# Optimization experiments

Hardware: AMD Instinct MI355X
Metric: run time of the kernel (lower is better)

## Reference

```python
import jax, jax.numpy as jnp
import numpy as np

B = 8
N_GENES = 19836
D_IN = 11
D_H = 64
DEG = 16
N = B * N_GENES
E_PER = N_GENES * DEG


def setup_inputs() -> dict:
    key = jax.random.key(0)
    ks = jax.random.split(key, 20)
    x = jax.random.normal(ks[0], (B, N_GENES, D_IN), dtype=jnp.float32)
    # edges: random within each graph, offset by graph index
    base_src = jax.random.randint(ks[1], (B, E_PER), 0, N_GENES)
    base_dst = jax.random.randint(ks[2], (B, E_PER), 0, N_GENES)
    offs = (jnp.arange(B) * N_GENES)[:, None]
    src = (base_src + offs).reshape(-1).astype(jnp.int64) if False else (base_src + offs).reshape(-1)
    dst = (base_dst + offs).reshape(-1)
    s = 0.02
    def nrm(k, shape):
        return jax.random.normal(k, shape, dtype=jnp.float32) * s
    return {
        'x': x, 'src': src, 'dst': dst,
        'enc_W': nrm(ks[3], (D_H, D_IN)), 'enc_b': jnp.zeros((D_H,), jnp.float32),
        'gene_emb': nrm(ks[4], (N_GENES, D_H)),
        'gin_W': nrm(ks[5], (D_H, D_H)),
        'bn_w': 1.0 + nrm(ks[6], (D_H,)), 'bn_b': jnp.zeros((D_H,), jnp.float32),
        'key_W': nrm(ks[7], (D_H, D_H)), 'key_b': jnp.zeros((D_H,), jnp.float32),
        'query_w': nrm(ks[8], (1, D_H)),
        'val_W': nrm(ks[9], (D_H, D_H)), 'val_b': jnp.zeros((D_H,), jnp.float32),
        'sae_enc_W': nrm(ks[10], (D_H, D_H)), 'sae_enc_b': jnp.zeros((D_H,), jnp.float32),
        'sae_dec_W': nrm(ks[11], (D_H, D_H)), 'sae_dec_b': jnp.zeros((D_H,), jnp.float32),
        'pred_W1': nrm(ks[12], (D_H, D_H)), 'pred_b1': jnp.zeros((D_H,), jnp.float32),
        'pred_W2': nrm(ks[13], (1, D_H)), 'pred_b2': jnp.zeros((1,), jnp.float32),
    }


def gelu(x):
    return jax.nn.gelu(x, approximate=False)  # nn.GELU default = exact erf


def batchnorm(h, w, b, eps=1e-5):
    # training-mode BatchNorm1d: batch statistics, biased variance
    mu = jnp.mean(h, axis=0)
    var = jnp.mean((h - mu) ** 2, axis=0)
    return (h - mu) * jax.lax.rsqrt(var + eps) * w + b


def reference(x, src, dst, enc_W, enc_b, gene_emb, gin_W, bn_w, bn_b,
              key_W, key_b, query_w, val_W, val_b,
              sae_enc_W, sae_enc_b, sae_dec_W, sae_dec_b,
              pred_W1, pred_b1, pred_W2, pred_b2):
    bsz, n_gene, d_in = x.shape
    n_nodes = bsz * n_gene
    # gene encoder: single Linear (bias) + GELU (inner batchnorm result is discarded in source)
    h = gelu(x.reshape(-1, d_in) @ enc_W.T + enc_b)          # [N, D_H]
    h = (h.reshape(bsz, n_gene, -1) + gene_emb).reshape(n_nodes, -1)
    # GIN layer (eps=0, sum aggregation): MLP(h + sum_{u->v} h_u); MLP = single Linear, no bias
    agg = jax.ops.segment_sum(h[src], dst, num_segments=n_nodes)  # irregular gather/scatter
    h = (h + agg) @ gin_W.T
    h = gelu(batchnorm(h, bn_w, bn_b))
    # attentive readout with SAE
    keys = h @ key_W.T + key_b
    w = jax.nn.sigmoid(keys @ query_w.T)                     # [N, 1]
    v = h @ val_W.T + val_b
    z = v * w
    enc = jax.nn.relu(z @ sae_enc_W.T + sae_enc_b)
    dec = enc @ sae_dec_W.T + sae_dec_b
    sae_loss = jnp.mean((dec - z) ** 2) + 1.0 * jnp.mean(jnp.abs(enc))
    gid = jnp.arange(n_nodes) // n_gene
    g_h = jax.ops.segment_sum(dec * w, gid, num_segments=bsz)  # [B, D_H]
    # predictor: Linear+GELU, Linear (inner batchnorm discarded in source)
    preds = gelu(g_h @ pred_W1.T + pred_b1) @ pred_W2.T + pred_b2
    return preds, w, sae_loss, dec
```

## Files before the change

kernel.cpp:

```cpp
#include <hip/hip_runtime.h>
#include <hip/hip_bf16.h>
#include <math.h>

#define NGENES 19836
#define BATCH 8
#define DIN 11
#define DH 64
#define NNODES (BATCH * NGENES)
#define E_PER (NGENES * 16)
#define NEDGES (NNODES * 16)
#define NDH (NNODES * DH)
#define NWAVE ((NNODES + 63) / 64)
#define NBLK_NODE ((NWAVE + 3) / 4)

#define SCAN_CHUNK 1024
#define NSBLK ((NNODES + SCAN_CHUNK - 1) / SCAN_CHUNK)

#define OUT_PREDS 0
#define OUT_W 8
#define OUT_SAE (8 + NNODES)
#define OUT_DEC (9 + NNODES)

__device__ __forceinline__ float gelu_f(float x) {
    return 0.5f * x * (1.0f + erff(x * 0.70710678118654752f));
}

__device__ __forceinline__ float bcast(float v, int lane) {
    return __int_as_float(__builtin_amdgcn_readlane(__float_as_int(v), lane));
}

__device__ __forceinline__ float wave_sum(float v) {
    #pragma unroll
    for (int o = 32; o; o >>= 1) v += __shfl_xor(v, o, 64);
    return v;
}

__global__ void k_encoder(const float* __restrict__ x, const float* __restrict__ encW,
                          const float* __restrict__ encB, const float* __restrict__ gemb,
                          __hip_bfloat16* __restrict__ h16) {
    int lane = threadIdx.x & 63;
    int g = blockIdx.x & 7;
    int wix = (blockIdx.x >> 3) * (blockDim.x >> 6) + (threadIdx.x >> 6);
    int wper = (gridDim.x >> 3) * (blockDim.x >> 6);
    float wreg[DIN];
    #pragma unroll
    for (int k = 0; k < DIN; ++k) wreg[k] = encW[lane * DIN + k];
    float bias = encB[lane];
    size_t gb = (size_t)g * NGENES;
    for (int i = wix; i < NGENES; i += wper) {
        size_t node = gb + i;
        const float* xr = x + node * DIN;
        float acc = bias;
        #pragma unroll
        for (int k = 0; k < DIN; ++k) acc = fmaf(xr[k], wreg[k], acc);
        float hv = gelu_f(acc) + gemb[(size_t)i * DH + lane];
        h16[node * DH + lane] = __float2bfloat16(hv);
    }
}

__global__ void k_hist(const int* __restrict__ dst, int* __restrict__ counts) {
    int g = blockIdx.x & 7;
    int t = (blockIdx.x >> 3) * blockDim.x + threadIdx.x;
    int nt = (gridDim.x >> 3) * blockDim.x;
    const int* dg = dst + (size_t)g * E_PER;
    for (int e = t; e < E_PER; e += nt)
        atomicAdd(&counts[dg[e]], 1);
}

__global__ void k_scan1(const int* __restrict__ counts, int* __restrict__ bsum) {
    __shared__ int red[256];
    int base = blockIdx.x * SCAN_CHUNK + threadIdx.x * 4;
    int s = 0;
    #pragma unroll
    for (int i = 0; i < 4; ++i) {
        int n = base + i;
        if (n < NNODES) s += counts[n];
    }
    red[threadIdx.x] = s;
    __syncthreads();
    for (int o = 128; o; o >>= 1) {
        if (threadIdx.x < o) red[threadIdx.x] += red[threadIdx.x + o];
        __syncthreads();
    }
    if (threadIdx.x == 0) bsum[blockIdx.x] = red[0];
}

__global__ void k_scan2(const int* __restrict__ bsum, int* __restrict__ boff) {
    __shared__ int red[256];
    int t = threadIdx.x;
    int v = (t < NSBLK) ? bsum[t] : 0;
    red[t] = v;
    __syncthreads();
    for (int o = 1; o < 256; o <<= 1) {
        int u = (t >= o) ? red[t - o] : 0;
        __syncthreads();
        red[t] += u;
        __syncthreads();
    }
    if (t < NSBLK) boff[t] = red[t] - v;
}

__global__ void k_scan3(const int* __restrict__ counts, const int* __restrict__ boff,
                        int* __restrict__ offsets, int* __restrict__ cursor) {
    __shared__ int red[256];
    int t = threadIdx.x;
    int base = blockIdx.x * SCAN_CHUNK + t * 4;
    int c[4];
    int s = 0;
    #pragma unroll
    for (int i = 0; i < 4; ++i) {
        int n = base + i;
        c[i] = (n < NNODES) ? counts[n] : 0;
        s += c[i];
    }
    red[t] = s;
    __syncthreads();
    for (int o = 1; o < 256; o <<= 1) {
        int v = (t >= o) ? red[t - o] : 0;
        __syncthreads();
        red[t] += v;
        __syncthreads();
    }
    int excl = red[t] - s + boff[blockIdx.x];
    #pragma unroll
    for (int i = 0; i < 4; ++i) {
        int n = base + i;
        if (n < NNODES) { offsets[n] = excl; cursor[n] = excl; }
        excl += c[i];
    }
}

__global__ void k_scatter(const int* __restrict__ src, const int* __restrict__ dst,
                          int* __restrict__ cursor, unsigned short* __restrict__ csr) {
    int g = blockIdx.x & 7;
    int t = (blockIdx.x >> 3) * blockDim.x + threadIdx.x;
    int nt = (gridDim.x >> 3) * blockDim.x;
    const int* sg = src + (size_t)g * E_PER;
    const int* dg = dst + (size_t)g * E_PER;
    int gbase = g * NGENES;
    for (int e = t; e < E_PER; e += nt) {
        int p = atomicAdd(&cursor[dg[e]], 1);
        csr[p] = (unsigned short)(sg[e] - gbase);
    }
}

__global__ void __launch_bounds__(256, 4)
k_aggin(const __hip_bfloat16* __restrict__ h16, const int* __restrict__ offsets,
        const int* __restrict__ counts, const unsigned short* __restrict__ csr,
        const float* __restrict__ ginW, float* __restrict__ h2,
        float* __restrict__ stats) {
    __shared__ float ldsW[DH * DH];
    __shared__ float red[2][256];
    for (int idx = threadIdx.x; idx < DH * DH; idx += 256) {
        int k = idx >> 6, d = idx & 63;
        ldsW[idx] = ginW[d * DH + k];
    }
    __syncthreads();
    int lane = threadIdx.x & 63;
    int g = blockIdx.x & 7;
    int wix = (blockIdx.x >> 3) * 4 + (threadIdx.x >> 6);
    int wper = (gridDim.x >> 3) * 4;
    int gbase = g * NGENES;
    float s1 = 0.f, s2 = 0.f;
    for (int i = wix; i < NGENES; i += wper) {
        int node = gbase + i;
        float a[8];
        a[0] = __bfloat162float(h16[(size_t)node * DH + lane]);
        #pragma unroll
        for (int u = 1; u < 8; ++u) a[u] = 0.f;
        int start = offsets[node];
        int cnt = counts[node];
        for (int e0 = 0; e0 < cnt; e0 += 64) {
            int nn = min(64, cnt - e0);
            int iv = (lane < nn) ? (int)csr[start + e0 + lane] : 0;
            int j = 0;
            for (; j + 7 < nn; j += 8) {
                #pragma unroll
                for (int u = 0; u < 8; ++u) {
                    int v = gbase + __shfl(iv, j + u, 64);
                    a[u] += __bfloat162float(h16[(size_t)v * DH + lane]);
                }
            }
            for (; j < nn; ++j)
                a[0] += __bfloat162float(h16[(size_t)(gbase + __shfl(iv, j, 64)) * DH + lane]);
        }
        float tval = ((a[0] + a[1]) + (a[2] + a[3])) + ((a[4] + a[5]) + (a[6] + a[7]));
        float m0 = 0.f, m1 = 0.f, m2 = 0.f, m3 = 0.f;
        #pragma unroll
        for (int k = 0; k < DH; k += 4) {
            m0 = fmaf(ldsW[(k + 0) * DH + lane], bcast(tval, k + 0), m0);
            m1 = fmaf(ldsW[(k + 1) * DH + lane], bcast(tval, k + 1), m1);
            m2 = fmaf(ldsW[(k + 2) * DH + lane], bcast(tval, k + 2), m2);
            m3 = fmaf(ldsW[(k + 3) * DH + lane], bcast(tval, k + 3), m3);
        }
        float outv = (m0 + m1) + (m2 + m3);
        h2[(size_t)node * DH + lane] = outv;
        s1 += outv;
        s2 += outv * outv;
    }
    red[0][threadIdx.x] = s1;
    red[1][threadIdx.x] = s2;
    __syncthreads();
    if (threadIdx.x < 64) {
        float t1 = red[0][threadIdx.x] + red[0][threadIdx.x + 64] + red[0][threadIdx.x + 128] + red[0][threadIdx.x + 192];
        float t2 = red[1][threadIdx.x] + red[1][threadIdx.x + 64] + red[1][threadIdx.x + 128] + red[1][threadIdx.x + 192];
        atomicAdd(&stats[threadIdx.x], t1);
        atomicAdd(&stats[64 + threadIdx.x], t2);
    }
}

__global__ void k_bnparams(const float* __restrict__ stats, const float* __restrict__ bnw,
                           const float* __restrict__ bnb, const float* __restrict__ keyW,
                           const float* __restrict__ keyB, const float* __restrict__ qw,
                           float* __restrict__ bnp) {
    int d = threadIdx.x;
    float inv_n = 1.0f / (float)NNODES;
    float mu = stats[d] * inv_n;
    float var = stats[64 + d] * inv_n - mu * mu;
    float sc = bnw[d] * rsqrtf(var + 1e-5f);
    bnp[d] = sc;
    bnp[64 + d] = bnb[d] - mu * sc;
    float kq0 = 0.f, kq1 = 0.f;
    #pragma unroll
    for (int j = 0; j < DH; j += 2) {
        kq0 = fmaf(qw[j], keyW[j * DH + d], kq0);
        kq1 = fmaf(qw[j + 1], keyW[(j + 1) * DH + d], kq1);
    }
    bnp[128 + d] = kq0 + kq1;
    float qb = wave_sum(qw[d] * keyB[d]);
    if (d == 0) bnp[192] = qb;
}

__global__ void __launch_bounds__(256, 2)
k_attn(float* __restrict__ h2, const float* __restrict__ bnp,
       const float* __restrict__ valW, const float* __restrict__ valB,
       float* __restrict__ wout) {
    int lane = threadIdx.x & 63;
    int wv = (blockIdx.x * blockDim.x + threadIdx.x) >> 6;
    int node = wv * 64 + lane;
    if (node >= NNODES) return;
    float* row = h2 + (size_t)node * DH;
    float h3[DH];
    #pragma unroll
    for (int j = 0; j < 16; ++j) {
        float4 v = *reinterpret_cast<const float4*>(row + j * 4);
        h3[j * 4] = v.x; h3[j * 4 + 1] = v.y; h3[j * 4 + 2] = v.z; h3[j * 4 + 3] = v.w;
    }
    float p = bnp[192];
    #pragma unroll
    for (int k = 0; k < DH; ++k) {
        h3[k] = gelu_f(fmaf(h3[k], bnp[k], bnp[64 + k]));
        p = fmaf(h3[k], bnp[128 + k], p);
    }
    float wq = 1.0f / (1.0f + expf(-p));
    wout[node] = wq;
    #pragma unroll 1
    for (int d4 = 0; d4 < DH; d4 += 4) {
        float a0 = valB[d4], a1 = valB[d4 + 1], a2 = valB[d4 + 2], a3 = valB[d4 + 3];
        #pragma unroll
        for (int k = 0; k < DH; ++k) {
            a0 = fmaf(valW[(d4 + 0) * DH + k], h3[k], a0);
            a1 = fmaf(valW[(d4 + 1) * DH + k], h3[k], a1);
            a2 = fmaf(valW[(d4 + 2) * DH + k], h3[k], a2);
            a3 = fmaf(valW[(d4 + 3) * DH + k], h3[k], a3);
        }
        float4 v = { a0 * wq, a1 * wq, a2 * wq, a3 * wq };
        *reinterpret_cast<float4*>(row + d4) = v;
    }
}

__global__ void __launch_bounds__(256, 2)
k_saenc(const float* __restrict__ zbuf, const float* __restrict__ encW,
        const float* __restrict__ encB, float* __restrict__ encout,
        float* __restrict__ loss) {
    int lane = threadIdx.x & 63;
    int wv = (blockIdx.x * blockDim.x + threadIdx.x) >> 6;
    int node = wv * 64 + lane;
    bool act = node < NNODES;
    const float* zr = zbuf + (size_t)node * DH;
    float z[DH];
    if (act) {
        #pragma unroll
        for (int j = 0; j < 16; ++j) {
            float4 v = *reinterpret_cast<const float4*>(zr + j * 4);
            z[j * 4] = v.x; z[j * 4 + 1] = v.y; z[j * 4 + 2] = v.z; z[j * 4 + 3] = v.w;
        }
    } else {
        #pragma unroll
        for (int k = 0; k < DH; ++k) z[k] = 0.f;
    }
    float l1 = 0.f;
    float* er = encout + (size_t)node * DH;
    #pragma unroll 1
    for (int d4 = 0; d4 < DH; d4 += 4) {
        float a0 = encB[d4], a1 = encB[d4 + 1], a2 = encB[d4 + 2], a3 = encB[d4 + 3];
        #pragma unroll
        for (int k = 0; k < DH; ++k) {
            a0 = fmaf(encW[(d4 + 0) * DH + k], z[k], a0);
            a1 = fmaf(encW[(d4 + 1) * DH + k], z[k], a1);
            a2 = fmaf(encW[(d4 + 2) * DH + k], z[k], a2);
            a3 = fmaf(encW[(d4 + 3) * DH + k], z[k], a3);
        }
        a0 = fmaxf(a0, 0.f); a1 = fmaxf(a1, 0.f);
        a2 = fmaxf(a2, 0.f); a3 = fmaxf(a3, 0.f);
        l1 += (a0 + a1) + (a2 + a3);
        if (act) {
            float4 v = { a0, a1, a2, a3 };
            *reinterpret_cast<float4*>(er + d4) = v;
        }
    }
    if (!act) l1 = 0.f;
    l1 = wave_sum(l1);
    if (lane == 0) atomicAdd(&loss[1], l1);
}

__global__ void __launch_bounds__(256, 2)
k_saedec(const float* __restrict__ zbuf, const float* __restrict__ decW,
         const float* __restrict__ decB, float* __restrict__ decout,
         float* __restrict__ loss) {
    int lane = threadIdx.x & 63;
    int wv = (blockIdx.x * blockDim.x + threadIdx.x) >> 6;
    int node = wv * 64 + lane;
    bool act = node < NNODES;
    float* dr = decout + (size_t)node * DH;
    const float* zr = zbuf + (size_t)node * DH;
    float enc[DH];
    if (act) {
        #pragma unroll
        for (int j = 0; j < 16; ++j) {
            float4 v = *reinterpret_cast<const float4*>(dr + j * 4);
            enc[j * 4] = v.x; enc[j * 4 + 1] = v.y; enc[j * 4 + 2] = v.z; enc[j * 4 + 3] = v.w;
        }
    } else {
        #pragma unroll
        for (int k = 0; k < DH; ++k) enc[k] = 0.f;
    }
    float sq = 0.f;
    #pragma unroll 1
    for (int d4 = 0; d4 < DH; d4 += 4) {
        float a0 = decB[d4], a1 = decB[d4 + 1], a2 = decB[d4 + 2], a3 = decB[d4 + 3];
        #pragma unroll
        for (int k = 0; k < DH; ++k) {
            a0 = fmaf(decW[(d4 + 0) * DH + k], enc[k], a0);
            a1 = fmaf(decW[(d4 + 1) * DH + k], enc[k], a1);
            a2 = fmaf(decW[(d4 + 2) * DH + k], enc[k], a2);
            a3 = fmaf(decW[(d4 + 3) * DH + k], enc[k], a3);
        }
        if (act) {
            float4 zv = *reinterpret_cast<const float4*>(zr + d4);
            float d0 = a0 - zv.x, d1 = a1 - zv.y, d2 = a2 - zv.z, d3 = a3 - zv.w;
            sq += (d0 * d0 + d1 * d1) + (d2 * d2 + d3 * d3);
            float4 v = { a0, a1, a2, a3 };
            *reinterpret_cast<float4*>(dr + d4) = v;
        }
    }
    sq = wave_sum(sq);
    if (lane == 0) atomicAdd(&loss[0], sq);
}

__global__ void k_ghsum(const float* __restrict__ dec, const float* __restrict__ wout,
                        float* __restrict__ g_h) {
    int lane = threadIdx.x & 63;
    int wid = (blockIdx.x * blockDim.x + threadIdx.x) >> 6;
    int tw = (gridDim.x * blockDim.x) >> 6;
    int chunk = (NNODES + tw - 1) / tw;
    int gs = wid * chunk;
    int ge = min(gs + chunk, NNODES);
    if (gs >= ge) return;
    float gacc = 0.f;
    int cur_g = gs / NGENES;
    for (int n = gs; n < ge; ++n) {
        int g = n / NGENES;
        if (g != cur_g) {
            atomicAdd(&g_h[cur_g * DH + lane], gacc);
            gacc = 0.f;
            cur_g = g;
        }
        gacc = fmaf(dec[(size_t)n * DH + lane], wout[n], gacc);
    }
    atomicAdd(&g_h[cur_g * DH + lane], gacc);
}

__global__ void k_pred(const float* __restrict__ g_h, const float* __restrict__ W1,
                       const float* __restrict__ b1, const float* __restrict__ W2,
                       const float* __restrict__ b2, const float* __restrict__ loss,
                       float* __restrict__ out) {
    int lane = threadIdx.x;
    float w1[DH];
    #pragma unroll
    for (int k = 0; k < DH; ++k) w1[k] = W1[lane * DH + k];
    float bb = b1[lane], w2 = W2[lane];
    for (int g = 0; g < BATCH; ++g) {
        float gh = g_h[g * DH + lane];
        float a0 = 0.f, a1 = 0.f;
        #pragma unroll
        for (int k = 0; k < DH; k += 2) {
            a0 = fmaf(w1[k], bcast(gh, k), a0);
            a1 = fmaf(w1[k + 1], bcast(gh, k + 1), a1);
        }
        float t = gelu_f(a0 + a1 + bb);
        float p = wave_sum(t * w2);
        if (lane == 0) out[OUT_PREDS + g] = p + b2[0];
    }
    if (lane == 0) out[OUT_SAE] = (loss[0] + loss[1]) * (1.0f / ((float)NNODES * (float)DH));
}

extern "C" void kernel_launch(void* const* d_in, const int* in_sizes, int n_in,
                              void* d_out, int out_size, void* d_ws, size_t ws_size,
                              hipStream_t stream) {
    const float* x    = (const float*)d_in[0];
    const int* src    = (const int*)d_in[1];
    const int* dst    = (const int*)d_in[2];
    const float* encW = (const float*)d_in[3];
    const float* encB = (const float*)d_in[4];
    const float* gemb = (const float*)d_in[5];
    const float* ginW = (const float*)d_in[6];
    const float* bnw  = (const float*)d_in[7];
    const float* bnb  = (const float*)d_in[8];
    const float* keyW = (const float*)d_in[9];
    const float* keyB = (const float*)d_in[10];
    const float* qw   = (const float*)d_in[11];
    const float* valW = (const float*)d_in[12];
    const float* valB = (const float*)d_in[13];
    const float* saeEncW = (const float*)d_in[14];
    const float* saeEncB = (const float*)d_in[15];
    const float* saeDecW = (const float*)d_in[16];
    const float* saeDecB = (const float*)d_in[17];
    const float* pW1  = (const float*)d_in[18];
    const float* pb1  = (const float*)d_in[19];
    const float* pW2  = (const float*)d_in[20];
    const float* pb2  = (const float*)d_in[21];

    float* out = (float*)d_out;
    float* ws = (float*)d_ws;

    int*   counts  = (int*)ws;
    float* stats   = ws + NNODES;
    float* g_h     = stats + 128;
    float* loss    = g_h + 512;
    float* bnp     = loss + 2;
    int*   offsets = (int*)(bnp + 256);
    int*   cursor  = offsets + NNODES;
    unsigned short* csr = (unsigned short*)(cursor + NNODES);
    int*   bsum    = (int*)(csr + NEDGES);
    int*   boff    = bsum + 256;
    float* h2      = (float*)(boff + 256);

    __hip_bfloat16* h16 = (__hip_bfloat16*)(out + OUT_DEC);
    float* decregion = out + OUT_DEC;
    float* wout = out + OUT_W;

    hipMemsetAsync(d_ws, 0, (size_t)(NNODES + 642) * sizeof(float), stream);

    k_encoder<<<2048, 256, 0, stream>>>(x, encW, encB, gemb, h16);
    k_hist<<<2048, 256, 0, stream>>>(dst, counts);
    k_scan1<<<NSBLK, 256, 0, stream>>>(counts, bsum);
    k_scan2<<<1, 256, 0, stream>>>(bsum, boff);
    k_scan3<<<NSBLK, 256, 0, stream>>>(counts, boff, offsets, cursor);
    k_scatter<<<2048, 256, 0, stream>>>(src, dst, cursor, csr);
    k_aggin<<<2048, 256, 0, stream>>>(h16, offsets, counts, csr, ginW, h2, stats);
    k_bnparams<<<1, 64, 0, stream>>>(stats, bnw, bnb, keyW, keyB, qw, bnp);
    k_attn<<<NBLK_NODE, 256, 0, stream>>>(h2, bnp, valW, valB, wout);
    k_saenc<<<NBLK_NODE, 256, 0, stream>>>(h2, saeEncW, saeEncB, decregion, loss);
    k_saedec<<<NBLK_NODE, 256, 0, stream>>>(h2, saeDecW, saeDecB, decregion, loss);
    k_ghsum<<<512, 256, 0, stream>>>(decregion, wout, g_h);
    k_pred<<<1, 64, 0, stream>>>(g_h, pW1, pb1, pW2, pb2, loss, out);
}
```

Before: 812.3 us.

## Fuse attention, SAE encoder/decoder and graph readout into one LDS-tiled kernel

Replaces four per-node kernels (attention/value, SAE encode, SAE decode, graph sum) with a single kernel. Each wave stages its 64-node tile in padded LDS with coalesced loads, keeps intermediates in registers or LDS, writes dec back coalesced, and does the per-graph weighted sum from LDS. This removes several full passes over the N×64 buffer in global memory and the strided per-lane row accesses. The cost is a large LDS footprint per block (about 66 KB), which may limit occupancy.

```diff
diff --git a/kernel.cpp b/kernel.cpp
--- a/kernel.cpp
+++ b/kernel.cpp
@@ -11,7 +11,8 @@
 #define NEDGES (NNODES * 16)
 #define NDH (NNODES * DH)
 #define NWAVE ((NNODES + 63) / 64)
-#define NBLK_NODE ((NWAVE + 3) / 4)
+#define NBLK_POST ((NWAVE + 3) / 4)
+#define TPAD 65
 
 #define SCAN_CHUNK 1024
 #define NSBLK ((NNODES + SCAN_CHUNK - 1) / SCAN_CHUNK)
@@ -232,153 +233,139 @@
 }
 
 __global__ void __launch_bounds__(256, 2)
-k_attn(float* __restrict__ h2, const float* __restrict__ bnp,
+k_post(const float* __restrict__ h2, const float* __restrict__ bnp,
        const float* __restrict__ valW, const float* __restrict__ valB,
-       float* __restrict__ wout) {
+       const float* __restrict__ encW, const float* __restrict__ encB,
+       const float* __restrict__ decW, const float* __restrict__ decB,
+       float* __restrict__ decout, float* __restrict__ wout,
+       float* __restrict__ g_h, float* __restrict__ loss) {
+    __shared__ float tile[4][64 * TPAD];
+    __shared__ float wqs[4][64];
     int lane = threadIdx.x & 63;
-    int wv = (blockIdx.x * blockDim.x + threadIdx.x) >> 6;
-    int node = wv * 64 + lane;
-    if (node >= NNODES) return;
-    float* row = h2 + (size_t)node * DH;
-    float h3[DH];
-    #pragma unroll
-    for (int j = 0; j < 16; ++j) {
-        float4 v = *reinterpret_cast<const float4*>(row + j * 4);
-        h3[j * 4] = v.x; h3[j * 4 + 1] = v.y; h3[j * 4 + 2] = v.z; h3[j * 4 + 3] = v.w;
-    }
+    int w = threadIdx.x >> 6;
+    int wg = blockIdx.x * 4 + w;
+    int tn = wg * 64;
+    if (tn >= NNODES) return;
+    float* T = tile[w];
+
+    {
+        const float* srcp = h2 + (size_t)tn * DH;
+        #pragma unroll
+        for (int j = 0; j < 16; ++j) {
+            int fid = j * 64 + lane;
+            int r = fid >> 4, c = (fid & 15) * 4;
+            float4 v = make_float4(0.f, 0.f, 0.f, 0.f);
+            if (tn + r < NNODES)
+                v = *reinterpret_cast<const float4*>(srcp + (size_t)fid * 4);
+            float* d = T + r * TPAD + c;
+            d[0] = v.x; d[1] = v.y; d[2] = v.z; d[3] = v.w;
+        }
+    }
+    __builtin_amdgcn_wave_barrier();
+
+    int node = tn + lane;
+    bool act = node < NNODES;
+    float* row = T + lane * TPAD;
+    float v64[DH];
+
     float p = bnp[192];
     #pragma unroll
     for (int k = 0; k < DH; ++k) {
-        h3[k] = gelu_f(fmaf(h3[k], bnp[k], bnp[64 + k]));
-        p = fmaf(h3[k], bnp[128 + k], p);
+        float hv = gelu_f(fmaf(row[k], bnp[k], bnp[64 + k]));
+        v64[k] = hv;
+        p = fmaf(hv, bnp[128 + k], p);
     }
     float wq = 1.0f / (1.0f + expf(-p));
-    wout[node] = wq;
+    if (act) wout[node] = wq;
+    wqs[w][lane] = act ? wq : 0.f;
+
     #pragma unroll 1
     for (int d4 = 0; d4 < DH; d4 += 4) {
         float a0 = valB[d4], a1 = valB[d4 + 1], a2 = valB[d4 + 2], a3 = valB[d4 + 3];
         #pragma unroll
         for (int k = 0; k < DH; ++k) {
-            a0 = fmaf(valW[(d4 + 0) * DH + k], h3[k], a0);
-            a1 = fmaf(valW[(d4 + 1) * DH + k], h3[k], a1);
-            a2 = fmaf(valW[(d4 + 2) * DH + k], h3[k], a2);
-            a3 = fmaf(valW[(d4 + 3) * DH + k], h3[k], a3);
-        }
-        float4 v = { a0 * wq, a1 * wq, a2 * wq, a3 * wq };
-        *reinterpret_cast<float4*>(row + d4) = v;
-    }
-}
-
-__global__ void __launch_bounds__(256, 2)
-k_saenc(const float* __restrict__ zbuf, const float* __restrict__ encW,
-        const float* __restrict__ encB, float* __restrict__ encout,
-        float* __restrict__ loss) {
-    int lane = threadIdx.x & 63;
-    int wv = (blockIdx.x * blockDim.x + threadIdx.x) >> 6;
-    int node = wv * 64 + lane;
-    bool act = node < NNODES;
-    const float* zr = zbuf + (size_t)node * DH;
-    float z[DH];
-    if (act) {
-        #pragma unroll
-        for (int j = 0; j < 16; ++j) {
-            float4 v = *reinterpret_cast<const float4*>(zr + j * 4);
-            z[j * 4] = v.x; z[j * 4 + 1] = v.y; z[j * 4 + 2] = v.z; z[j * 4 + 3] = v.w;
-        }
-    } else {
-        #pragma unroll
-        for (int k = 0; k < DH; ++k) z[k] = 0.f;
-    }
+            float hk = v64[k];
+            a0 = fmaf(valW[(d4 + 0) * DH + k], hk, a0);
+            a1 = fmaf(valW[(d4 + 1) * DH + k], hk, a1);
+            a2 = fmaf(valW[(d4 + 2) * DH + k], hk, a2);
+            a3 = fmaf(valW[(d4 + 3) * DH + k], hk, a3);
+        }
+        row[d4 + 0] = a0 * wq; row[d4 + 1] = a1 * wq;
+        row[d4 + 2] = a2 * wq; row[d4 + 3] = a3 * wq;
+    }
+
     float l1 = 0.f;
-    float* er = encout + (size_t)node * DH;
     #pragma unroll 1
     for (int d4 = 0; d4 < DH; d4 += 4) {
         float a0 = encB[d4], a1 = encB[d4 + 1], a2 = encB[d4 + 2], a3 = encB[d4 + 3];
         #pragma unroll
         for (int k = 0; k < DH; ++k) {
-            a0 = fmaf(encW[(d4 + 0) * DH + k], z[k], a0);
-            a1 = fmaf(encW[(d4 + 1) * DH + k], z[k], a1);
-            a2 = fmaf(encW[(d4 + 2) * DH + k], z[k], a2);
-            a3 = fmaf(encW[(d4 + 3) * DH + k], z[k], a3);
+            float zk = row[k];
+            a0 = fmaf(encW[(d4 + 0) * DH + k], zk, a0);
+            a1 = fmaf(encW[(d4 + 1) * DH + k], zk, a1);
+            a2 = fmaf(encW[(d4 + 2) * DH + k], zk, a2);
+            a3 = fmaf(encW[(d4 + 3) * DH + k], zk, a3);
         }
         a0 = fmaxf(a0, 0.f); a1 = fmaxf(a1, 0.f);
         a2 = fmaxf(a2, 0.f); a3 = fmaxf(a3, 0.f);
         l1 += (a0 + a1) + (a2 + a3);
-        if (act) {
-            float4 v = { a0, a1, a2, a3 };
-            *reinterpret_cast<float4*>(er + d4) = v;
-        }
-    }
-    if (!act) l1 = 0.f;
-    l1 = wave_sum(l1);
-    if (lane == 0) atomicAdd(&loss[1], l1);
-}
-
-__global__ void __launch_bounds__(256, 2)
-k_saedec(const float* __restrict__ zbuf, const float* __restrict__ decW,
-         const float* __restrict__ decB, float* __restrict__ decout,
-         float* __restrict__ loss) {
-    int lane = threadIdx.x & 63;
-    int wv = (blockIdx.x * blockDim.x + threadIdx.x) >> 6;
-    int node = wv * 64 + lane;
-    bool act = node < NNODES;
-    float* dr = decout + (size_t)node * DH;
-    const float* zr = zbuf + (size_t)node * DH;
-    float enc[DH];
-    if (act) {
-        #pragma unroll
-        for (int j = 0; j < 16; ++j) {
-            float4 v = *reinterpret_cast<const float4*>(dr + j * 4);
-            enc[j * 4] = v.x; enc[j * 4 + 1] = v.y; enc[j * 4 + 2] = v.z; enc[j * 4 + 3] = v.w;
-        }
-    } else {
-        #pragma unroll
-        for (int k = 0; k < DH; ++k) enc[k] = 0.f;
-    }
+        v64[d4 + 0] = a0; v64[d4 + 1] = a1; v64[d4 + 2] = a2; v64[d4 + 3] = a3;
+    }
+
     float sq = 0.f;
     #pragma unroll 1
     for (int d4 = 0; d4 < DH; d4 += 4) {
         float a0 = decB[d4], a1 = decB[d4 + 1], a2 = decB[d4 + 2], a3 = decB[d4 + 3];
         #pragma unroll
         for (int k = 0; k < DH; ++k) {
-            a0 = fmaf(decW[(d4 + 0) * DH + k], enc[k], a0);
-            a1 = fmaf(decW[(d4 + 1) * DH + k], enc[k], a1);
-            a2 = fmaf(decW[(d4 + 2) * DH + k], enc[k], a2);
-            a3 = fmaf(decW[(d4 + 3) * DH + k], enc[k], a3);
-        }
-        if (act) {
-            float4 zv = *reinterpret_cast<const float4*>(zr + d4);
-            float d0 = a0 - zv.x, d1 = a1 - zv.y, d2 = a2 - zv.z, d3 = a3 - zv.w;
-            sq += (d0 * d0 + d1 * d1) + (d2 * d2 + d3 * d3);
-            float4 v = { a0, a1, a2, a3 };
-            *reinterpret_cast<float4*>(dr + d4) = v;
-        }
-    }
+            float ek = v64[k];
+            a0 = fmaf(decW[(d4 + 0) * DH + k], ek, a0);
+            a1 = fmaf(decW[(d4 + 1) * DH + k], ek, a1);
+            a2 = fmaf(decW[(d4 + 2) * DH + k], ek, a2);
+            a3 = fmaf(decW[(d4 + 3) * DH + k], ek, a3);
+        }
+        float z0 = row[d4 + 0], z1 = row[d4 + 1], z2 = row[d4 + 2], z3 = row[d4 + 3];
+        float e0 = a0 - z0, e1 = a1 - z1, e2 = a2 - z2, e3 = a3 - z3;
+        sq += (e0 * e0 + e1 * e1) + (e2 * e2 + e3 * e3);
+        row[d4 + 0] = a0; row[d4 + 1] = a1; row[d4 + 2] = a2; row[d4 + 3] = a3;
+    }
+    __builtin_amdgcn_wave_barrier();
+
+    {
+        float* dstp = decout + (size_t)tn * DH;
+        #pragma unroll
+        for (int j = 0; j < 16; ++j) {
+            int fid = j * 64 + lane;
+            int r = fid >> 4, c = (fid & 15) * 4;
+            if (tn + r < NNODES) {
+                const float* s = T + r * TPAD + c;
+                float4 v = { s[0], s[1], s[2], s[3] };
+                *reinterpret_cast<float4*>(dstp + (size_t)fid * 4) = v;
+            }
+        }
+    }
+
+    {
+        int g0 = tn / NGENES;
+        int bnd = (g0 + 1) * NGENES - tn;
+        if (bnd > 64) bnd = 64;
+        float acc0 = 0.f, acc1 = 0.f;
+        for (int r = 0; r < 64; ++r) {
+            float v = T[r * TPAD + lane] * wqs[w][r];
+            if (r < bnd) acc0 += v; else acc1 += v;
+        }
+        atomicAdd(&g_h[g0 * DH + lane], acc0);
+        if (bnd < 64 && g0 + 1 < BATCH)
+            atomicAdd(&g_h[(g0 + 1) * DH + lane], acc1);
+    }
+
+    if (!act) { l1 = 0.f; sq = 0.f; }
     sq = wave_sum(sq);
-    if (lane == 0) atomicAdd(&loss[0], sq);
-}
-
-__global__ void k_ghsum(const float* __restrict__ dec, const float* __restrict__ wout,
-                        float* __restrict__ g_h) {
-    int lane = threadIdx.x & 63;
-    int wid = (blockIdx.x * blockDim.x + threadIdx.x) >> 6;
-    int tw = (gridDim.x * blockDim.x) >> 6;
-    int chunk = (NNODES + tw - 1) / tw;
-    int gs = wid * chunk;
-    int ge = min(gs + chunk, NNODES);
-    if (gs >= ge) return;
-    float gacc = 0.f;
-    int cur_g = gs / NGENES;
-    for (int n = gs; n < ge; ++n) {
-        int g = n / NGENES;
-        if (g != cur_g) {
-            atomicAdd(&g_h[cur_g * DH + lane], gacc);
-            gacc = 0.f;
-            cur_g = g;
-        }
-        gacc = fmaf(dec[(size_t)n * DH + lane], wout[n], gacc);
-    }
-    atomicAdd(&g_h[cur_g * DH + lane], gacc);
+    l1 = wave_sum(l1);
+    if (lane == 0) {
+        atomicAdd(&loss[0], sq);
+        atomicAdd(&loss[1], l1);
+    }
 }
 
 __global__ void k_pred(const float* __restrict__ g_h, const float* __restrict__ W1,
@@ -460,9 +447,8 @@
     k_scatter<<<2048, 256, 0, stream>>>(src, dst, cursor, csr);
     k_aggin<<<2048, 256, 0, stream>>>(h16, offsets, counts, csr, ginW, h2, stats);
     k_bnparams<<<1, 64, 0, stream>>>(stats, bnw, bnb, keyW, keyB, qw, bnp);
-    k_attn<<<NBLK_NODE, 256, 0, stream>>>(h2, bnp, valW, valB, wout);
-    k_saenc<<<NBLK_NODE, 256, 0, stream>>>(h2, saeEncW, saeEncB, decregion, loss);
-    k_saedec<<<NBLK_NODE, 256, 0, stream>>>(h2, saeDecW, saeDecB, decregion, loss);
-    k_ghsum<<<512, 256, 0, stream>>>(decregion, wout, g_h);
+    k_post<<<NBLK_POST, 256, 0, stream>>>(h2, bnp, valW, valB,
+                                          saeEncW, saeEncB, saeDecW, saeDecB,
+                                          decregion, wout, g_h, loss);
     k_pred<<<1, 64, 0, stream>>>(g_h, pW1, pb1, pW2, pb2, loss, out);
 }
```

New measurement: 828.1 us. Within noise of the previous version (+1.9%).

## Fuse attention, SAE encoder and decoder into one per-node kernel with prefolded weights

Applied to the files above, without the earlier changes.

Merges the three per-node kernels (value projection + attention weight, SAE encode, SAE decode) into a single kernel so the z and enc intermediates stay in registers instead of going through global memory. A small prologue kernel precomputes saeEncW·valW and saeEncW·valB, letting the encoder run directly on h3, with the scalar weight applied afterwards. The value projection is still recomputed inside the decoder loop to form z for the MSE term. This removes two full 64-wide round trips through HBM and two launches, at the cost of more registers and extra FMAs per node.

```diff
diff --git a/kernel.cpp b/kernel.cpp
--- a/kernel.cpp
+++ b/kernel.cpp
@@ -10,8 +10,7 @@
 #define E_PER (NGENES * 16)
 #define NEDGES (NNODES * 16)
 #define NDH (NNODES * DH)
-#define NWAVE ((NNODES + 63) / 64)
-#define NBLK_NODE ((NWAVE + 3) / 4)
+#define NBLK_POST ((NNODES + 255) / 256)
 
 #define SCAN_CHUNK 1024
 #define NSBLK ((NNODES + SCAN_CHUNK - 1) / SCAN_CHUNK)
@@ -55,6 +54,26 @@
         for (int k = 0; k < DIN; ++k) acc = fmaf(xr[k], wreg[k], acc);
         float hv = gelu_f(acc) + gemb[(size_t)i * DH + lane];
         h16[node * DH + lane] = __float2bfloat16(hv);
+    }
+}
+
+__global__ void k_prew(const float* __restrict__ encW, const float* __restrict__ valW,
+                       const float* __restrict__ valB, float* __restrict__ M1,
+                       float* __restrict__ m1v) {
+    int tid = threadIdx.x;
+    for (int e = tid; e < DH * DH; e += 256) {
+        int d = e >> 6, k = e & 63;
+        float acc = 0.f;
+        #pragma unroll 4
+        for (int j = 0; j < DH; ++j)
+            acc = fmaf(encW[d * DH + j], valW[j * DH + k], acc);
+        M1[e] = acc;
+    }
+    if (tid < DH) {
+        float acc = 0.f;
+        for (int j = 0; j < DH; ++j)
+            acc = fmaf(encW[tid * DH + j], valB[j], acc);
+        m1v[tid] = acc;
     }
 }
 
@@ -232,130 +251,91 @@
 }
 
 __global__ void __launch_bounds__(256, 2)
-k_attn(float* __restrict__ h2, const float* __restrict__ bnp,
+k_post(const float* __restrict__ h2, const float* __restrict__ bnp,
        const float* __restrict__ valW, const float* __restrict__ valB,
-       float* __restrict__ wout) {
+       const float* __restrict__ M1, const float* __restrict__ m1v,
+       const float* __restrict__ encB,
+       const float* __restrict__ decW, const float* __restrict__ decB,
+       float* __restrict__ decout, float* __restrict__ wout,
+       float* __restrict__ loss) {
     int lane = threadIdx.x & 63;
-    int wv = (blockIdx.x * blockDim.x + threadIdx.x) >> 6;
-    int node = wv * 64 + lane;
-    if (node >= NNODES) return;
-    float* row = h2 + (size_t)node * DH;
+    int node = blockIdx.x * 256 + threadIdx.x;
+    bool act = node < NNODES;
+    int nc = act ? node : 0;
+
+    const float* srcp = h2 + (size_t)nc * DH;
     float h3[DH];
     #pragma unroll
     for (int j = 0; j < 16; ++j) {
-        float4 v = *reinterpret_cast<const float4*>(row + j * 4);
-        h3[j * 4] = v.x; h3[j * 4 + 1] = v.y; h3[j * 4 + 2] = v.z; h3[j * 4 + 3] = v.w;
+        float4 v = *reinterpret_cast<const float4*>(srcp + j * 4);
+        h3[j * 4 + 0] = v.x; h3[j * 4 + 1] = v.y;
+        h3[j * 4 + 2] = v.z; h3[j * 4 + 3] = v.w;
     }
     float p = bnp[192];
     #pragma unroll
     for (int k = 0; k < DH; ++k) {
-        h3[k] = gelu_f(fmaf(h3[k], bnp[k], bnp[64 + k]));
-        p = fmaf(h3[k], bnp[128 + k], p);
+        float hv = gelu_f(fmaf(h3[k], bnp[k], bnp[64 + k]));
+        h3[k] = hv;
+        p = fmaf(hv, bnp[128 + k], p);
     }
     float wq = 1.0f / (1.0f + expf(-p));
-    wout[node] = wq;
+    if (act) wout[node] = wq;
+
+    float enc[DH];
+    float l1 = 0.f;
     #pragma unroll 1
     for (int d4 = 0; d4 < DH; d4 += 4) {
-        float a0 = valB[d4], a1 = valB[d4 + 1], a2 = valB[d4 + 2], a3 = valB[d4 + 3];
+        float a0 = 0.f, a1 = 0.f, a2 = 0.f, a3 = 0.f;
         #pragma unroll
         for (int k = 0; k < DH; ++k) {
-            a0 = fmaf(valW[(d4 + 0) * DH + k], h3[k], a0);
-            a1 = fmaf(valW[(d4 + 1) * DH + k], h3[k], a1);
-            a2 = fmaf(valW[(d4 + 2) * DH + k], h3[k], a2);
-            a3 = fmaf(valW[(d4 + 3) * DH + k], h3[k], a3);
-        }
-        float4 v = { a0 * wq, a1 * wq, a2 * wq, a3 * wq };
-        *reinterpret_cast<float4*>(row + d4) = v;
-    }
-}
-
-__global__ void __launch_bounds__(256, 2)
-k_saenc(const float* __restrict__ zbuf, const float* __restrict__ encW,
-        const float* __restrict__ encB, float* __restrict__ encout,
-        float* __restrict__ loss) {
-    int lane = threadIdx.x & 63;
-    int wv = (blockIdx.x * blockDim.x + threadIdx.x) >> 6;
-    int node = wv * 64 + lane;
-    bool act = node < NNODES;
-    const float* zr = zbuf + (size_t)node * DH;
-    float z[DH];
-    if (act) {
-        #pragma unroll
-        for (int j = 0; j < 16; ++j) {
-            float4 v = *reinterpret_cast<const float4*>(zr + j * 4);
-            z[j * 4] = v.x; z[j * 4 + 1] = v.y; z[j * 4 + 2] = v.z; z[j * 4 + 3] = v.w;
-        }
-    } else {
-        #pragma unroll
-        for (int k = 0; k < DH; ++k) z[k] = 0.f;
-    }
-    float l1 = 0.f;
-    float* er = encout + (size_t)node * DH;
+            float hk = h3[k];
+            a0 = fmaf(M1[(d4 + 0) * DH + k], hk, a0);
+            a1 = fmaf(M1[(d4 + 1) * DH + k], hk, a1);
+            a2 = fmaf(M1[(d4 + 2) * DH + k], hk, a2);
+            a3 = fmaf(M1[(d4 + 3) * DH + k], hk, a3);
+        }
+        a0 = fmaxf(fmaf(wq, a0 + m1v[d4 + 0], encB[d4 + 0]), 0.f);
+        a1 = fmaxf(fmaf(wq, a1 + m1v[d4 + 1], encB[d4 + 1]), 0.f);
+        a2 = fmaxf(fmaf(wq, a2 + m1v[d4 + 2], encB[d4 + 2]), 0.f);
+        a3 = fmaxf(fmaf(wq, a3 + m1v[d4 + 3], encB[d4 + 3]), 0.f);
+        l1 += (a0 + a1) + (a2 + a3);
+        enc[d4 + 0] = a0; enc[d4 + 1] = a1; enc[d4 + 2] = a2; enc[d4 + 3] = a3;
+    }
+
+    float sq = 0.f;
+    float* dr = decout + (size_t)nc * DH;
     #pragma unroll 1
     for (int d4 = 0; d4 < DH; d4 += 4) {
-        float a0 = encB[d4], a1 = encB[d4 + 1], a2 = encB[d4 + 2], a3 = encB[d4 + 3];
+        float b0 = decB[d4 + 0], b1 = decB[d4 + 1], b2 = decB[d4 + 2], b3 = decB[d4 + 3];
+        float c0 = valB[d4 + 0], c1 = valB[d4 + 1], c2 = valB[d4 + 2], c3 = valB[d4 + 3];
         #pragma unroll
         for (int k = 0; k < DH; ++k) {
-            a0 = fmaf(encW[(d4 + 0) * DH + k], z[k], a0);
-            a1 = fmaf(encW[(d4 + 1) * DH + k], z[k], a1);
-            a2 = fmaf(encW[(d4 + 2) * DH + k], z[k], a2);
-            a3 = fmaf(encW[(d4 + 3) * DH + k], z[k], a3);
-        }
-        a0 = fmaxf(a0, 0.f); a1 = fmaxf(a1, 0.f);
-        a2 = fmaxf(a2, 0.f); a3 = fmaxf(a3, 0.f);
-        l1 += (a0 + a1) + (a2 + a3);
+            float ek = enc[k], hk = h3[k];
+            b0 = fmaf(decW[(d4 + 0) * DH + k], ek, b0);
+            b1 = fmaf(decW[(d4 + 1) * DH + k], ek, b1);
+            b2 = fmaf(decW[(d4 + 2) * DH + k], ek, b2);
+            b3 = fmaf(decW[(d4 + 3) * DH + k], ek, b3);
+            c0 = fmaf(valW[(d4 + 0) * DH + k], hk, c0);
+            c1 = fmaf(valW[(d4 + 1) * DH + k], hk, c1);
+            c2 = fmaf(valW[(d4 + 2) * DH + k], hk, c2);
+            c3 = fmaf(valW[(d4 + 3) * DH + k], hk, c3);
+        }
+        c0 *= wq; c1 *= wq; c2 *= wq; c3 *= wq;
+        float e0 = b0 - c0, e1 = b1 - c1, e2 = b2 - c2, e3 = b3 - c3;
+        sq += (e0 * e0 + e1 * e1) + (e2 * e2 + e3 * e3);
         if (act) {
-            float4 v = { a0, a1, a2, a3 };
-            *reinterpret_cast<float4*>(er + d4) = v;
-        }
-    }
-    if (!act) l1 = 0.f;
+            float4 v = { b0, b1, b2, b3 };
+            *reinterpret_cast<float4*>(dr + d4) = v;
+        }
+    }
+
+    if (!act) { sq = 0.f; l1 = 0.f; }
+    sq = wave_sum(sq);
     l1 = wave_sum(l1);
-    if (lane == 0) atomicAdd(&loss[1], l1);
-}
-
-__global__ void __launch_bounds__(256, 2)
-k_saedec(const float* __restrict__ zbuf, const float* __restrict__ decW,
-         const float* __restrict__ decB, float* __restrict__ decout,
-         float* __restrict__ loss) {
-    int lane = threadIdx.x & 63;
-    int wv = (blockIdx.x * blockDim.x + threadIdx.x) >> 6;
-    int node = wv * 64 + lane;
-    bool act = node < NNODES;
-    float* dr = decout + (size_t)node * DH;
-    const float* zr = zbuf + (size_t)node * DH;
-    float enc[DH];
-    if (act) {
-        #pragma unroll
-        for (int j = 0; j < 16; ++j) {
-            float4 v = *reinterpret_cast<const float4*>(dr + j * 4);
-            enc[j * 4] = v.x; enc[j * 4 + 1] = v.y; enc[j * 4 + 2] = v.z; enc[j * 4 + 3] = v.w;
-        }
-    } else {
-        #pragma unroll
-        for (int k = 0; k < DH; ++k) enc[k] = 0.f;
-    }
-    float sq = 0.f;
-    #pragma unroll 1
-    for (int d4 = 0; d4 < DH; d4 += 4) {
-        float a0 = decB[d4], a1 = decB[d4 + 1], a2 = decB[d4 + 2], a3 = decB[d4 + 3];
-        #pragma unroll
-        for (int k = 0; k < DH; ++k) {
-            a0 = fmaf(decW[(d4 + 0) * DH + k], enc[k], a0);
-            a1 = fmaf(decW[(d4 + 1) * DH + k], enc[k], a1);
-            a2 = fmaf(decW[(d4 + 2) * DH + k], enc[k], a2);
-            a3 = fmaf(decW[(d4 + 3) * DH + k], enc[k], a3);
-        }
-        if (act) {
-            float4 zv = *reinterpret_cast<const float4*>(zr + d4);
-            float d0 = a0 - zv.x, d1 = a1 - zv.y, d2 = a2 - zv.z, d3 = a3 - zv.w;
-            sq += (d0 * d0 + d1 * d1) + (d2 * d2 + d3 * d3);
-            float4 v = { a0, a1, a2, a3 };
-            *reinterpret_cast<float4*>(dr + d4) = v;
-        }
-    }
-    sq = wave_sum(sq);
-    if (lane == 0) atomicAdd(&loss[0], sq);
+    if (lane == 0) {
+        atomicAdd(&loss[0], sq);
+        atomicAdd(&loss[1], l1);
+    }
 }
 
 __global__ void k_ghsum(const float* __restrict__ dec, const float* __restrict__ wout,
@@ -439,7 +419,9 @@
     float* g_h     = stats + 128;
     float* loss    = g_h + 512;
     float* bnp     = loss + 2;
-    int*   offsets = (int*)(bnp + 256);
+    float* M1      = bnp + 256;
+    float* m1v     = M1 + 4096;
+    int*   offsets = (int*)(m1v + 64);
     int*   cursor  = offsets + NNODES;
     unsigned short* csr = (unsigned short*)(cursor + NNODES);
     int*   bsum    = (int*)(csr + NEDGES);
@@ -452,6 +434,7 @@
 
     hipMemsetAsync(d_ws, 0, (size_t)(NNODES + 642) * sizeof(float), stream);
 
+    k_prew<<<1, 256, 0, stream>>>(saeEncW, valW, valB, M1, m1v);
     k_encoder<<<2048, 256, 0, stream>>>(x, encW, encB, gemb, h16);
     k_hist<<<2048, 256, 0, stream>>>(dst, counts);
     k_scan1<<<NSBLK, 256, 0, stream>>>(counts, bsum);
@@ -460,9 +443,9 @@
     k_scatter<<<2048, 256, 0, stream>>>(src, dst, cursor, csr);
     k_aggin<<<2048, 256, 0, stream>>>(h16, offsets, counts, csr, ginW, h2, stats);
     k_bnparams<<<1, 64, 0, stream>>>(stats, bnw, bnb, keyW, keyB, qw, bnp);
-    k_attn<<<NBLK_NODE, 256, 0, stream>>>(h2, bnp, valW, valB, wout);
-    k_saenc<<<NBLK_NODE, 256, 0, stream>>>(h2, saeEncW, saeEncB, decregion, loss);
-    k_saedec<<<NBLK_NODE, 256, 0, stream>>>(h2, saeDecW, saeDecB, decregion, loss);
+    k_post<<<NBLK_POST, 256, 0, stream>>>(h2, bnp, valW, valB, M1, m1v,
+                                          saeEncB, saeDecW, saeDecB,
+                                          decregion, wout, loss);
     k_ghsum<<<512, 256, 0, stream>>>(decregion, wout, g_h);
     k_pred<<<1, 64, 0, stream>>>(g_h, pW1, pb1, pW2, pb2, loss, out);
 }
```

After: 995.0 us. 22.5% more time.
